# Kernel optimization log

Hardware: AMD Instinct MI355X
Metric: run time of the kernel (lower is better)

Reference implementation:

```python
import jax, jax.numpy as jnp
import numpy as np

B, N, C = 8, 1025, 768  # batch, tokens (1 CLS + 32*32 patches), channels
H = 12                  # heads
D = C // H              # head dim = 64
EPS = 1e-6

def _rot(x):
    # stack([-x[..., 1::2], x[..., ::2]], -1).reshape(x.shape)
    return jnp.stack([-x[..., 1::2], x[..., ::2]], axis=-1).reshape(x.shape)

def apply_rot_embed_cat(x, emb):
    # emb: [N-1, 2*D] = concat(sin, cos); x: [B, H, N-1, D]
    sin, cos = jnp.split(emb, 2, axis=-1)
    return x * cos + _rot(x) * sin

def setup_inputs() -> dict:
    key = jax.random.key(0)
    ks = jax.random.split(key, 8)
    s = 0.02
    return {
        "x": jax.random.normal(ks[0], (B, N, C), jnp.float32),
        "rope": jax.random.normal(ks[1], (N - 1, 2 * D), jnp.float32),
        "w_qkv": jax.random.normal(ks[2], (C, 3 * C), jnp.float32) * s,
        "q_bias": jax.random.normal(ks[3], (C,), jnp.float32) * s,
        "v_bias": jax.random.normal(ks[4], (C,), jnp.float32) * s,
        "gamma": jnp.ones((C,), jnp.float32),
        "beta": jnp.zeros((C,), jnp.float32),
        "w_proj": jax.random.normal(ks[5], (C, C), jnp.float32) * s,
        "b_proj": jnp.zeros((C,), jnp.float32),
    }

def reference(x, rope, w_qkv, q_bias, v_bias, gamma, beta, w_proj, b_proj):
    scale = D ** (-0.5)
    qkv_bias = jnp.concatenate([q_bias, jnp.zeros_like(q_bias), v_bias], axis=0)
    qkv = x @ w_qkv + qkv_bias  # [B, N, 3C]
    qkv = qkv.reshape(B, N, 3, H, D).transpose(2, 0, 3, 1, 4)  # [3, B, H, N, D]
    q, k, v = qkv[0], qkv[1], qkv[2]
    # RoPE on non-CLS tokens only
    q = jnp.concatenate([q[:, :, :1], apply_rot_embed_cat(q[:, :, 1:], rope)], axis=2)
    k = jnp.concatenate([k[:, :, :1], apply_rot_embed_cat(k[:, :, 1:], rope)], axis=2)
    attn = jnp.einsum('bhqd,bhkd->bhqk', q * scale, k)
    attn = jax.nn.softmax(attn, axis=-1)
    y = jnp.einsum('bhqk,bhkd->bhqd', attn, v)
    y = y.transpose(0, 2, 1, 3).reshape(B, N, C)
    # LayerNorm
    mu = jnp.mean(y, axis=-1, keepdims=True)
    var = jnp.mean(jnp.square(y - mu), axis=-1, keepdims=True)
    y = (y - mu) * jax.lax.rsqrt(var + EPS) * gamma + beta
    return y @ w_proj + b_proj
```

## Files before the change

### kernel.cpp

```cpp
#include <hip/hip_runtime.h>

typedef __bf16 bf16_t;
typedef __bf16 bf16x8 __attribute__((ext_vector_type(8)));
typedef float f32x4 __attribute__((ext_vector_type(4)));
typedef float f32x16 __attribute__((ext_vector_type(16)));
typedef unsigned short u16;
typedef unsigned int u32;

#define NTOK 1025
#define MTOT 8200
#define MPAD 8448
#define CDIM 768

#define GLOAD(dst, p) \
  asm volatile("global_load_dwordx4 %0, %1, off" : "=&v"(dst) : "v"((const void*)(p)))

__device__ __forceinline__ u16 f2bf(float f) {
  union { float f; unsigned u; } v; v.f = f;
  unsigned r = v.u + 0x7fffu + ((v.u >> 16) & 1u);
  return (u16)(r >> 16);
}
__device__ __forceinline__ float bf2f(u16 h) {
  union { unsigned u; float f; } v; v.u = ((unsigned)h) << 16; return v.f;
}
__device__ __forceinline__ u32 cvtpk(float lo, float hi) {
  u32 r; asm("v_cvt_pk_bf16_f32 %0, %1, %2" : "=v"(r) : "v"(lo), "v"(hi)); return r;
}

__global__ __launch_bounds__(256) void conv_xf(const float4* __restrict__ x4,
                                               u16* __restrict__ xf) {
  __shared__ u16 tile[16][776];
  int mt = blockIdx.x;
  int t = threadIdx.x;
#pragma unroll
  for (int it = 0; it < 12; ++it) {
    int id = it * 256 + t;
    int r = id / 192, c4 = id % 192;
    int m = mt * 16 + r;
    if (m < MTOT) {
      float4 f = x4[(size_t)m * 192 + c4];
      ushort4 o; o.x = f2bf(f.x); o.y = f2bf(f.y); o.z = f2bf(f.z); o.w = f2bf(f.w);
      *(ushort4*)&tile[r][c4 * 4] = o;
    }
  }
  __syncthreads();
#pragma unroll
  for (int it = 0; it < 6; ++it) {
    int cid = it * 256 + t;
    int kt = cid >> 6, lane = cid & 63;
    uint4 w = *(const uint4*)&tile[lane & 15][kt * 32 + (lane >> 4) * 8];
    *(uint4*)&xf[(((size_t)mt * 24 + kt) * 64 + lane) * 8] = w;
  }
}

__global__ __launch_bounds__(64) void transp_wf(const float* __restrict__ in, int N,
                                                u16* __restrict__ wf) {
  __shared__ u16 lds[16][32];
  int n0 = blockIdx.x * 16, k0 = blockIdx.y * 32;
  int t = threadIdx.x;
#pragma unroll
  for (int it = 0; it < 8; ++it) {
    int e = it * 64 + t;
    int kk = e >> 4, nn = e & 15;
    lds[nn][kk] = f2bf(in[(size_t)(k0 + kk) * N + n0 + nn]);
  }
  __syncthreads();
  uint4 w = *(const uint4*)&lds[t & 15][(t >> 4) * 8];
  *(uint4*)&wf[((((size_t)(n0 >> 4)) * 24 + (k0 >> 5)) * 64 + t) * 8] = w;
}

template <bool TRANS>
__device__ __forceinline__ void fdloop(const u16* __restrict__ afr, const u16* __restrict__ bfr,
                                       int m0, int n0, int lane, int wr, int wc,
                                       f32x4 (*acc)[4]) {
  const u16* ab = afr + ((size_t)((m0 >> 4) + wr * 4) * 1536 + lane) * 8;
  const u16* bb = bfr + ((size_t)((n0 >> 4) + wc * 4) * 1536 + lane) * 8;
  bf16x8 S[3][8];
  auto LOADA = [&](int s, int kt) {
#pragma unroll
    for (int i = 0; i < 4; ++i)
      GLOAD(S[s][i], ab + (size_t)i * 12288 + (size_t)kt * 512);
#pragma unroll
    for (int j = 0; j < 4; ++j)
      GLOAD(S[s][4 + j], bb + (size_t)j * 12288 + (size_t)kt * 512);
  };
  auto COMP = [&](bf16x8 (&Sc)[8]) {
    __builtin_amdgcn_s_setprio(1);
#pragma unroll
    for (int x = 0; x < 4; ++x)
#pragma unroll
      for (int y = 0; y < 4; ++y)
        acc[x][y] = TRANS
            ? __builtin_amdgcn_mfma_f32_16x16x32_bf16(Sc[4 + x], Sc[y], acc[x][y], 0, 0, 0)
            : __builtin_amdgcn_mfma_f32_16x16x32_bf16(Sc[x], Sc[4 + y], acc[x][y], 0, 0, 0);
    __builtin_amdgcn_s_setprio(0);
  };
  LOADA(0, 0);
  LOADA(1, 1);
#pragma unroll
  for (int kt = 0; kt < 24; ++kt) {
    if (kt < 22) {
      LOADA((kt + 2) % 3, kt + 2);
      asm volatile("s_waitcnt vmcnt(16)");
    } else if (kt == 22) {
      asm volatile("s_waitcnt vmcnt(8)");
    } else {
      asm volatile("s_waitcnt vmcnt(0)");
    }
    __builtin_amdgcn_sched_barrier(0);
    COMP(S[kt % 3]);
  }
}

__global__ __launch_bounds__(256, 2) void qkv_gemm_t(
    const u16* __restrict__ xf, const u16* __restrict__ wf,
    const float* __restrict__ qbias, const float* __restrict__ rope,
    u16* __restrict__ q, u16* __restrict__ kfr) {
  const int NB = 12;
  int tau0 = blockIdx.x;
  int xcd = tau0 & 7, pos = tau0 >> 3;
  int tau = (xcd < 4) ? xcd * 98 + pos : 392 + (xcd - 4) * 97 + pos;
  int bx = tau % NB, by = tau / NB;
  int m0 = by * 128, n0 = bx * 128;
  int t = threadIdx.x;
  int lane = t & 63, wave = t >> 6;
  int ln = lane & 15, hi = lane >> 4;
  int wr = wave >> 1, wc = wave & 1;

  f32x4 acc[4][4] = {};
  fdloop<true>(xf, wf, m0, n0, lane, wr, wc, acc);

  const float scale = 0.125f * 1.4426950408889634f;
#pragma unroll
  for (int ii = 0; ii < 4; ++ii) {
    int m = m0 + wr * 64 + ii * 16 + ln;
    if (m < MTOT) {
      int b = m / NTOK;
      int n = m - b * NTOK;
      const float* rp = rope + (size_t)(n - 1) * 128;
#pragma unroll
      for (int jj = 0; jj < 4; ++jj) {
        int c4 = n0 + wc * 64 + jj * 16 + hi * 4;
        int part = (c4 >= CDIM) ? 1 : 0;
        int cc = c4 - part * CDIM;
        int h = cc >> 6, d4 = cc & 63;
        float v0 = acc[jj][ii][0], v1 = acc[jj][ii][1];
        float v2 = acc[jj][ii][2], v3 = acc[jj][ii][3];
        if (part == 0) {
          float4 qb = *(const float4*)(qbias + cc);
          v0 += qb.x; v1 += qb.y; v2 += qb.z; v3 += qb.w;
        }
        float o0, o1, o2, o3;
        if (n > 0) {
          float4 sn = *(const float4*)(rp + d4);
          float4 cs = *(const float4*)(rp + 64 + d4);
          o0 = v0 * cs.x - v1 * sn.x;
          o1 = v1 * cs.y + v0 * sn.y;
          o2 = v2 * cs.z - v3 * sn.z;
          o3 = v3 * cs.w + v2 * sn.w;
        } else { o0 = v0; o1 = v1; o2 = v2; o3 = v3; }
        uint2 w;
        if (part == 0) {
          w.x = cvtpk(o0 * scale, o1 * scale); w.y = cvtpk(o2 * scale, o3 * scale);
          *(uint2*)(q + ((size_t)(h * MPAD + m)) * 64 + d4) = w;
        } else {
          w.x = cvtpk(o0, o1); w.y = cvtpk(o2, o3);
          int kt2 = n >> 5, lqn = n & 31;
          int sF = d4 >> 4, h2d = (d4 >> 3) & 1, j0 = d4 & 7;
          u16* dst = kfr + ((((size_t)(h * 8 + b) * 34 + kt2) * 4 + sF) * 64
                            + h2d * 32 + lqn) * 8 + j0;
          *(uint2*)dst = w;
        }
      }
    }
  }
}

__global__ __launch_bounds__(256, 2) void qkv_gemm_v(
    const u16* __restrict__ xf, const u16* __restrict__ wf,
    const float* __restrict__ vbias, u16* __restrict__ vfr) {
  const int NB = 6;
  int tau0 = blockIdx.x;
  int xcd = tau0 & 7, pos = tau0 >> 3;
  int tau = (xcd < 6) ? xcd * 49 + pos : 294 + (xcd - 6) * 48 + pos;
  int bx = tau % NB, by = tau / NB;
  int m0 = by * 128, n0 = 1536 + bx * 128;
  int t = threadIdx.x;
  int lane = t & 63, wave = t >> 6;
  int ln = lane & 15, hi = lane >> 4;
  int wr = wave >> 1, wc = wave & 1;

  f32x4 acc[4][4] = {};
  fdloop<false>(xf, wf, m0, n0, lane, wr, wc, acc);

#pragma unroll
  for (int i = 0; i < 4; ++i) {
    int mrow = m0 + wr * 64 + i * 16 + hi * 4;
#pragma unroll
    for (int j = 0; j < 4; ++j) {
      int cv = n0 - 1536 + wc * 64 + j * 16 + ln;
      int h = cv >> 6, d = cv & 63;
      int hf = d >> 5, lqd = d & 31;
      float vb = vbias[cv];
#pragma unroll
      for (int r = 0; r < 4; ++r) {
        int mr = mrow + r;
        if (mr < MTOT) {
          int b = mr / NTOK;
          int n = mr - b * NTOK;
          size_t idx = ((((size_t)(h * 8 + b) * 17 + (n >> 6)) * 4 + ((n >> 4) & 3)) * 2 + hf) * 512
                     + (size_t)((((n >> 3) & 1) * 32 + lqd) * 8 + (n & 7));
          vfr[idx] = f2bf(acc[i][j][r] + vb);
        }
      }
    }
  }
}

template <bool PF, bool MASK>
__device__ __forceinline__ void flash_iter(
    bf16x8 (&kf)[8], bf16x8 (&kn)[8], int pftile, int it,
    const u16* kfb, const u16* vfb, int h2,
    const bf16x8 (&qf)[4], f32x16 (&acc)[2], float& l) {
  bf16x8 vf[8];
  const u16* vp2 = vfb + (size_t)it * 4096;
#pragma unroll
  for (int hf = 0; hf < 2; ++hf)
#pragma unroll
    for (int s = 0; s < 4; ++s)
      GLOAD(vf[hf * 4 + s], vp2 + (s * 2 + hf) * 512);
  if (PF) {
    const u16* kp2 = kfb + (size_t)pftile * 4096;
#pragma unroll
    for (int c = 0; c < 2; ++c)
#pragma unroll
      for (int s = 0; s < 4; ++s)
        GLOAD(kn[c * 4 + s], kp2 + c * 2048 + s * 512);
  }
  if (PF) asm volatile("s_waitcnt vmcnt(16)");
  else    asm volatile("s_waitcnt vmcnt(8)");
  __builtin_amdgcn_sched_barrier(0);
  f32x16 sc[2] = {};
  __builtin_amdgcn_s_setprio(1);
#pragma unroll
  for (int c = 0; c < 2; ++c)
#pragma unroll
    for (int s = 0; s < 4; ++s)
      sc[c] = __builtin_amdgcn_mfma_f32_32x32x16_bf16(kf[c * 4 + s], qf[s], sc[c], 0, 0, 0);
  __builtin_amdgcn_s_setprio(0);
#pragma unroll
  for (int c = 0; c < 2; ++c)
#pragma unroll
    for (int r = 0; r < 16; ++r)
      sc[c][r] = __builtin_amdgcn_exp2f(sc[c][r]);
  if (MASK) {
#pragma unroll
    for (int c = 0; c < 2; ++c)
#pragma unroll
      for (int r = 0; r < 16; ++r) {
        int kk = it * 64 + c * 32 + (r & 3) + 8 * (r >> 2) + 4 * h2;
        if (kk >= NTOK) sc[c][r] = 0.f;
      }
  }
  float rs = 0.f;
#pragma unroll
  for (int c = 0; c < 2; ++c)
#pragma unroll
    for (int r = 0; r < 16; ++r) rs += sc[c][r];
  l += rs;
  bf16x8 frag[4];
#pragma unroll
  for (int c = 0; c < 2; ++c) {
    u32 k0 = cvtpk(sc[c][0], sc[c][1]),   k1 = cvtpk(sc[c][2], sc[c][3]);
    u32 k2 = cvtpk(sc[c][4], sc[c][5]),   k3 = cvtpk(sc[c][6], sc[c][7]);
    u32 k4 = cvtpk(sc[c][8], sc[c][9]),   k5 = cvtpk(sc[c][10], sc[c][11]);
    u32 k6 = cvtpk(sc[c][12], sc[c][13]), k7 = cvtpk(sc[c][14], sc[c][15]);
    asm("v_permlane32_swap_b32 %0, %1" : "+v"(k0), "+v"(k2));
    asm("v_permlane32_swap_b32 %0, %1" : "+v"(k1), "+v"(k3));
    asm("v_permlane32_swap_b32 %0, %1" : "+v"(k4), "+v"(k6));
    asm("v_permlane32_swap_b32 %0, %1" : "+v"(k5), "+v"(k7));
    union { u32 u[4]; bf16x8 v; } u0, u1;
    u0.u[0] = k0; u0.u[1] = k1; u0.u[2] = k2; u0.u[3] = k3;
    u1.u[0] = k4; u1.u[1] = k5; u1.u[2] = k6; u1.u[3] = k7;
    frag[c * 2] = u0.v; frag[c * 2 + 1] = u1.v;
  }
  if (PF) asm volatile("s_waitcnt vmcnt(8)");
  else    asm volatile("s_waitcnt vmcnt(0)");
  __builtin_amdgcn_sched_barrier(0);
  __builtin_amdgcn_s_setprio(1);
#pragma unroll
  for (int hf = 0; hf < 2; ++hf)
#pragma unroll
    for (int s = 0; s < 4; ++s)
      acc[hf] = __builtin_amdgcn_mfma_f32_32x32x16_bf16(vf[hf * 4 + s], frag[s], acc[hf], 0, 0, 0);
  __builtin_amdgcn_s_setprio(0);
}

__global__ __launch_bounds__(256, 2) void flash_attn(
    const u16* __restrict__ q, const u16* __restrict__ kfr,
    const u16* __restrict__ vfr, u16* __restrict__ y) {
  int f = blockIdx.x;
  int xcd = f & 7, idx = f >> 3;
  int bh = xcd * 12 + idx / 9;
  int qt = idx - (idx / 9) * 9;
  int b = bh / 12, h = bh - b * 12;
  int t = threadIdx.x, lane = t & 63, w = t >> 6;
  int lq = lane & 31, h2 = lane >> 5;
  int q0 = qt * 128 + w * 32;
  if (q0 >= NTOK) return;
  int qrow = q0 + lq; if (qrow > NTOK - 1) qrow = NTOK - 1;

  const u16* qp = q + ((size_t)(h * MPAD) + (size_t)b * NTOK + qrow) * 64;
  bf16x8 qf[4];
#pragma unroll
  for (int s = 0; s < 4; ++s)
    qf[s] = *(const bf16x8*)&qp[s * 16 + h2 * 8];

  const u16* kfb = kfr + (size_t)(h * 8 + b) * 34 * 2048 + lane * 8;
  const u16* vfb = vfr + (size_t)(h * 8 + b) * 17 * 4096 + lane * 8;

  f32x16 acc[2] = {};
  float l = 0.f;

  bf16x8 ka[8], kb2[8];
#pragma unroll
  for (int c = 0; c < 2; ++c)
#pragma unroll
    for (int s = 0; s < 4; ++s)
      GLOAD(ka[c * 4 + s], kfb + c * 2048 + s * 512);

#pragma unroll 1
  for (int i2 = 0; i2 < 8; ++i2) {
    flash_iter<true, false>(ka, kb2, 2 * i2 + 1, 2 * i2, kfb, vfb, h2, qf, acc, l);
    flash_iter<true, false>(kb2, ka, 2 * i2 + 2, 2 * i2 + 1, kfb, vfb, h2, qf, acc, l);
  }
  flash_iter<false, true>(ka, kb2, 0, 16, kfb, vfb, h2, qf, acc, l);

  int row = q0 + lq;
  if (row < NTOK) {
    float lt = l + __shfl_xor(l, 32, 64);
    float inv = 1.f / lt;
    u16* yr = y + ((size_t)(b * NTOK + row)) * CDIM + h * 64;
#pragma unroll
    for (int hf = 0; hf < 2; ++hf)
#pragma unroll
      for (int g = 0; g < 4; ++g) {
        int d0 = hf * 32 + 8 * g + 4 * h2;
        ushort4 o;
        o.x = f2bf(acc[hf][g * 4 + 0] * inv);
        o.y = f2bf(acc[hf][g * 4 + 1] * inv);
        o.z = f2bf(acc[hf][g * 4 + 2] * inv);
        o.w = f2bf(acc[hf][g * 4 + 3] * inv);
        *(ushort4*)&yr[d0] = o;
      }
  }
}

__global__ __launch_bounds__(256) void lnorm(const u16* __restrict__ y,
                                             const float* __restrict__ gamma,
                                             const float* __restrict__ beta,
                                             u16* __restrict__ yf) {
  int row = blockIdx.x;
  const u16* yr = y + (size_t)row * CDIM;
  int t = threadIdx.x;
  float v[3];
  float s = 0.f, s2 = 0.f;
#pragma unroll
  for (int i = 0; i < 3; ++i) {
    v[i] = bf2f(yr[t + 256 * i]);
    s += v[i]; s2 += v[i] * v[i];
  }
#pragma unroll
  for (int msk = 1; msk < 64; msk <<= 1) {
    s  += __shfl_xor(s, msk, 64);
    s2 += __shfl_xor(s2, msk, 64);
  }
  __shared__ float ws[8];
  int w = t >> 6, lane = t & 63;
  if (lane == 0) { ws[w] = s; ws[4 + w] = s2; }
  __syncthreads();
  s = ws[0] + ws[1] + ws[2] + ws[3];
  s2 = ws[4] + ws[5] + ws[6] + ws[7];
  float mu = s * (1.f / 768.f);
  float var = s2 * (1.f / 768.f) - mu * mu;
  float rstd = rsqrtf(var + 1e-6f);
  if (t < 96) {
    union { uint4 u4; u16 u[8]; } iv, ov;
    iv.u4 = *(const uint4*)&yr[t * 8];
    const float* gp = gamma + t * 8;
    const float* bp = beta + t * 8;
#pragma unroll
    for (int j = 0; j < 8; ++j)
      ov.u[j] = f2bf((bf2f(iv.u[j]) - mu) * rstd * gp[j] + bp[j]);
    int kt = t >> 2, ln2 = (row & 15) + 16 * (t & 3), mt = row >> 4;
    *(uint4*)&yf[(((size_t)mt * 24 + kt) * 64 + ln2) * 8] = ov.u4;
  }
}

__global__ __launch_bounds__(256, 2) void proj_gemm(
    const u16* __restrict__ yf, const u16* __restrict__ wf,
    const float* __restrict__ bias, float* __restrict__ out) {
  const int NB = 6;
  int tau0 = blockIdx.x;
  int xcd = tau0 & 7, pos = tau0 >> 3;
  int tau = (xcd < 6) ? xcd * 49 + pos : 294 + (xcd - 6) * 48 + pos;
  int bx = tau % NB, by = tau / NB;
  int m0 = by * 128, n0 = bx * 128;
  int t = threadIdx.x;
  int lane = t & 63, wave = t >> 6;
  int ln = lane & 15, hi = lane >> 4;
  int wr = wave >> 1, wc = wave & 1;

  f32x4 acc[4][4] = {};
  fdloop<true>(yf, wf, m0, n0, lane, wr, wc, acc);

#pragma unroll
  for (int ii = 0; ii < 4; ++ii) {
    int m = m0 + wr * 64 + ii * 16 + ln;
    if (m < MTOT) {
      float* dr = out + (size_t)m * CDIM;
#pragma unroll
      for (int jj = 0; jj < 4; ++jj) {
        int c4 = n0 + wc * 64 + jj * 16 + hi * 4;
        float4 bv = *(const float4*)(bias + c4);
        float4 o;
        o.x = acc[jj][ii][0] + bv.x;
        o.y = acc[jj][ii][1] + bv.y;
        o.z = acc[jj][ii][2] + bv.z;
        o.w = acc[jj][ii][3] + bv.w;
        *(float4*)(dr + c4) = o;
      }
    }
  }
}

extern "C" void kernel_launch(void* const* d_in, const int* in_sizes, int n_in,
                              void* d_out, int out_size, void* d_ws, size_t ws_size,
                              hipStream_t stream) {
  const float* x      = (const float*)d_in[0];
  const float* rope   = (const float*)d_in[1];
  const float* w_qkv  = (const float*)d_in[2];
  const float* q_bias = (const float*)d_in[3];
  const float* v_bias = (const float*)d_in[4];
  const float* gamma  = (const float*)d_in[5];
  const float* beta   = (const float*)d_in[6];
  const float* w_proj = (const float*)d_in[7];
  const float* b_proj = (const float*)d_in[8];
  float* out = (float*)d_out;

  char* ws = (char*)d_ws;
  u16* xf   = (u16*)(ws);
  u16* ybf  = (u16*)(ws);
  u16* wfq  = (u16*)(ws + 12976128);
  u16* wfp  = (u16*)(ws + 16515072);
  u16* qbuf = (u16*)(ws + 17694720);
  u16* yf   = (u16*)(ws + 17694720);
  u16* kfr  = (u16*)(ws + 30670848);
  u16* vfr  = (u16*)(ws + 44040192);

  conv_xf<<<dim3(513), 256, 0, stream>>>((const float4*)x, xf);
  transp_wf<<<dim3(144, 24), 64, 0, stream>>>(w_qkv, 2304, wfq);
  transp_wf<<<dim3(48, 24), 64, 0, stream>>>(w_proj, 768, wfp);

  qkv_gemm_t<<<dim3(780), 256, 0, stream>>>(xf, wfq, q_bias, rope, qbuf, kfr);
  qkv_gemm_v<<<dim3(390), 256, 0, stream>>>(xf, wfq, v_bias, vfr);
  flash_attn<<<dim3(864), 256, 0, stream>>>(qbuf, kfr, vfr, ybf);
  lnorm<<<8200, 256, 0, stream>>>(ybf, gamma, beta, yf);
  proj_gemm<<<dim3(390), 256, 0, stream>>>(yf, wfp, b_proj, out);
}
```

Baseline: 171.2 us.

## Merge Q/K and V projection GEMMs into one launch; use compiler-scheduled loads in flash attention

Fuses the two QKV GEMM kernels into a single 1170-block launch that branches per tile on whether it produces Q/K (with bias and RoPE) or V, with an XCD remapping for the larger grid. This removes one kernel launch and the tail imbalance between the two grids. Separately, the flash-attention loop drops its inline-asm global loads and manual vmcnt waits in favour of plain vector loads, with the K prefetch issued before the V loads. That hands scheduling to the compiler and risks losing the hand-tuned overlap of memory and MFMA.

After: 159.7 us. 6.7% less time.

```diff
diff --git a/kernel.cpp b/kernel.cpp
--- a/kernel.cpp
+++ b/kernel.cpp
@@ -112,105 +112,95 @@
   }
 }
 
-__global__ __launch_bounds__(256, 2) void qkv_gemm_t(
+__global__ __launch_bounds__(256, 2) void qkv_gemm_all(
     const u16* __restrict__ xf, const u16* __restrict__ wf,
-    const float* __restrict__ qbias, const float* __restrict__ rope,
-    u16* __restrict__ q, u16* __restrict__ kfr) {
-  const int NB = 12;
+    const float* __restrict__ qbias, const float* __restrict__ vbias,
+    const float* __restrict__ rope,
+    u16* __restrict__ q, u16* __restrict__ kfr, u16* __restrict__ vfr) {
+  const int NB = 18;
   int tau0 = blockIdx.x;
   int xcd = tau0 & 7, pos = tau0 >> 3;
-  int tau = (xcd < 4) ? xcd * 98 + pos : 392 + (xcd - 4) * 97 + pos;
+  int tau = (xcd < 2) ? xcd * 147 + pos : 294 + (xcd - 2) * 146 + pos;
   int bx = tau % NB, by = tau / NB;
-  int m0 = by * 128, n0 = bx * 128;
+  int m0 = by * 128;
   int t = threadIdx.x;
   int lane = t & 63, wave = t >> 6;
   int ln = lane & 15, hi = lane >> 4;
   int wr = wave >> 1, wc = wave & 1;
 
-  f32x4 acc[4][4] = {};
-  fdloop<true>(xf, wf, m0, n0, lane, wr, wc, acc);
-
-  const float scale = 0.125f * 1.4426950408889634f;
-#pragma unroll
-  for (int ii = 0; ii < 4; ++ii) {
-    int m = m0 + wr * 64 + ii * 16 + ln;
-    if (m < MTOT) {
-      int b = m / NTOK;
-      int n = m - b * NTOK;
-      const float* rp = rope + (size_t)(n - 1) * 128;
-#pragma unroll
-      for (int jj = 0; jj < 4; ++jj) {
-        int c4 = n0 + wc * 64 + jj * 16 + hi * 4;
-        int part = (c4 >= CDIM) ? 1 : 0;
-        int cc = c4 - part * CDIM;
-        int h = cc >> 6, d4 = cc & 63;
-        float v0 = acc[jj][ii][0], v1 = acc[jj][ii][1];
-        float v2 = acc[jj][ii][2], v3 = acc[jj][ii][3];
-        if (part == 0) {
-          float4 qb = *(const float4*)(qbias + cc);
-          v0 += qb.x; v1 += qb.y; v2 += qb.z; v3 += qb.w;
-        }
-        float o0, o1, o2, o3;
-        if (n > 0) {
-          float4 sn = *(const float4*)(rp + d4);
-          float4 cs = *(const float4*)(rp + 64 + d4);
-          o0 = v0 * cs.x - v1 * sn.x;
-          o1 = v1 * cs.y + v0 * sn.y;
-          o2 = v2 * cs.z - v3 * sn.z;
-          o3 = v3 * cs.w + v2 * sn.w;
-        } else { o0 = v0; o1 = v1; o2 = v2; o3 = v3; }
-        uint2 w;
-        if (part == 0) {
-          w.x = cvtpk(o0 * scale, o1 * scale); w.y = cvtpk(o2 * scale, o3 * scale);
-          *(uint2*)(q + ((size_t)(h * MPAD + m)) * 64 + d4) = w;
-        } else {
-          w.x = cvtpk(o0, o1); w.y = cvtpk(o2, o3);
-          int kt2 = n >> 5, lqn = n & 31;
-          int sF = d4 >> 4, h2d = (d4 >> 3) & 1, j0 = d4 & 7;
-          u16* dst = kfr + ((((size_t)(h * 8 + b) * 34 + kt2) * 4 + sF) * 64
-                            + h2d * 32 + lqn) * 8 + j0;
-          *(uint2*)dst = w;
+  if (bx < 12) {
+    int n0 = bx * 128;
+    f32x4 acc[4][4] = {};
+    fdloop<true>(xf, wf, m0, n0, lane, wr, wc, acc);
+
+    const float scale = 0.125f * 1.4426950408889634f;
+#pragma unroll
+    for (int ii = 0; ii < 4; ++ii) {
+      int m = m0 + wr * 64 + ii * 16 + ln;
+      if (m < MTOT) {
+        int b = m / NTOK;
+        int n = m - b * NTOK;
+        const float* rp = rope + (size_t)(n - 1) * 128;
+#pragma unroll
+        for (int jj = 0; jj < 4; ++jj) {
+          int c4 = n0 + wc * 64 + jj * 16 + hi * 4;
+          int part = (c4 >= CDIM) ? 1 : 0;
+          int cc = c4 - part * CDIM;
+          int h = cc >> 6, d4 = cc & 63;
+          float v0 = acc[jj][ii][0], v1 = acc[jj][ii][1];
+          float v2 = acc[jj][ii][2], v3 = acc[jj][ii][3];
+          if (part == 0) {
+            float4 qb = *(const float4*)(qbias + cc);
+            v0 += qb.x; v1 += qb.y; v2 += qb.z; v3 += qb.w;
+          }
+          float o0, o1, o2, o3;
+          if (n > 0) {
+            float4 sn = *(const float4*)(rp + d4);
+            float4 cs = *(const float4*)(rp + 64 + d4);
+            o0 = v0 * cs.x - v1 * sn.x;
+            o1 = v1 * cs.y + v0 * sn.y;
+            o2 = v2 * cs.z - v3 * sn.z;
+            o3 = v3 * cs.w + v2 * sn.w;
+          } else { o0 = v0; o1 = v1; o2 = v2; o3 = v3; }
+          uint2 w;
+          if (part == 0) {
+            w.x = cvtpk(o0 * scale, o1 * scale); w.y = cvtpk(o2 * scale, o3 * scale);
+            *(uint2*)(q + ((size_t)(h * MPAD + m)) * 64 + d4) = w;
+          } else {
+            w.x = cvtpk(o0, o1); w.y = cvtpk(o2, o3);
+            int kt2 = n >> 5, lqn = n & 31;
+            int sF = d4 >> 4, h2d = (d4 >> 3) & 1, j0 = d4 & 7;
+            u16* dst = kfr + ((((size_t)(h * 8 + b) * 34 + kt2) * 4 + sF) * 64
+                              + h2d * 32 + lqn) * 8 + j0;
+            *(uint2*)dst = w;
+          }
         }
       }
     }
-  }
-}
-
-__global__ __launch_bounds__(256, 2) void qkv_gemm_v(
-    const u16* __restrict__ xf, const u16* __restrict__ wf,
-    const float* __restrict__ vbias, u16* __restrict__ vfr) {
-  const int NB = 6;
-  int tau0 = blockIdx.x;
-  int xcd = tau0 & 7, pos = tau0 >> 3;
-  int tau = (xcd < 6) ? xcd * 49 + pos : 294 + (xcd - 6) * 48 + pos;
-  int bx = tau % NB, by = tau / NB;
-  int m0 = by * 128, n0 = 1536 + bx * 128;
-  int t = threadIdx.x;
-  int lane = t & 63, wave = t >> 6;
-  int ln = lane & 15, hi = lane >> 4;
-  int wr = wave >> 1, wc = wave & 1;
-
-  f32x4 acc[4][4] = {};
-  fdloop<false>(xf, wf, m0, n0, lane, wr, wc, acc);
-
-#pragma unroll
-  for (int i = 0; i < 4; ++i) {
-    int mrow = m0 + wr * 64 + i * 16 + hi * 4;
-#pragma unroll
-    for (int j = 0; j < 4; ++j) {
-      int cv = n0 - 1536 + wc * 64 + j * 16 + ln;
-      int h = cv >> 6, d = cv & 63;
-      int hf = d >> 5, lqd = d & 31;
-      float vb = vbias[cv];
-#pragma unroll
-      for (int r = 0; r < 4; ++r) {
-        int mr = mrow + r;
-        if (mr < MTOT) {
-          int b = mr / NTOK;
-          int n = mr - b * NTOK;
-          size_t idx = ((((size_t)(h * 8 + b) * 17 + (n >> 6)) * 4 + ((n >> 4) & 3)) * 2 + hf) * 512
-                     + (size_t)((((n >> 3) & 1) * 32 + lqd) * 8 + (n & 7));
-          vfr[idx] = f2bf(acc[i][j][r] + vb);
+  } else {
+    int n0 = 1536 + (bx - 12) * 128;
+    f32x4 acc[4][4] = {};
+    fdloop<false>(xf, wf, m0, n0, lane, wr, wc, acc);
+
+#pragma unroll
+    for (int i = 0; i < 4; ++i) {
+      int mrow = m0 + wr * 64 + i * 16 + hi * 4;
+#pragma unroll
+      for (int j = 0; j < 4; ++j) {
+        int cv = n0 - 1536 + wc * 64 + j * 16 + ln;
+        int h = cv >> 6, d = cv & 63;
+        int hf = d >> 5, lqd = d & 31;
+        float vb = vbias[cv];
+#pragma unroll
+        for (int r = 0; r < 4; ++r) {
+          int mr = mrow + r;
+          if (mr < MTOT) {
+            int b = mr / NTOK;
+            int n = mr - b * NTOK;
+            size_t idx = ((((size_t)(h * 8 + b) * 17 + (n >> 6)) * 4 + ((n >> 4) & 3)) * 2 + hf) * 512
+                       + (size_t)((((n >> 3) & 1) * 32 + lqd) * 8 + (n & 7));
+            vfr[idx] = f2bf(acc[i][j][r] + vb);
+          }
         }
       }
     }
@@ -222,24 +212,21 @@
     bf16x8 (&kf)[8], bf16x8 (&kn)[8], int pftile, int it,
     const u16* kfb, const u16* vfb, int h2,
     const bf16x8 (&qf)[4], f32x16 (&acc)[2], float& l) {
+  if (PF) {
+    const u16* kp2 = kfb + (size_t)pftile * 4096;
+#pragma unroll
+    for (int c = 0; c < 2; ++c)
+#pragma unroll
+      for (int s = 0; s < 4; ++s)
+        kn[c * 4 + s] = *(const bf16x8*)(kp2 + c * 2048 + s * 512);
+  }
   bf16x8 vf[8];
   const u16* vp2 = vfb + (size_t)it * 4096;
 #pragma unroll
   for (int hf = 0; hf < 2; ++hf)
 #pragma unroll
     for (int s = 0; s < 4; ++s)
-      GLOAD(vf[hf * 4 + s], vp2 + (s * 2 + hf) * 512);
-  if (PF) {
-    const u16* kp2 = kfb + (size_t)pftile * 4096;
-#pragma unroll
-    for (int c = 0; c < 2; ++c)
-#pragma unroll
-      for (int s = 0; s < 4; ++s)
-        GLOAD(kn[c * 4 + s], kp2 + c * 2048 + s * 512);
-  }
-  if (PF) asm volatile("s_waitcnt vmcnt(16)");
-  else    asm volatile("s_waitcnt vmcnt(8)");
-  __builtin_amdgcn_sched_barrier(0);
+      vf[hf * 4 + s] = *(const bf16x8*)(vp2 + (s * 2 + hf) * 512);
   f32x16 sc[2] = {};
   __builtin_amdgcn_s_setprio(1);
 #pragma unroll
@@ -284,9 +271,6 @@
     u1.u[0] = k4; u1.u[1] = k5; u1.u[2] = k6; u1.u[3] = k7;
     frag[c * 2] = u0.v; frag[c * 2 + 1] = u1.v;
   }
-  if (PF) asm volatile("s_waitcnt vmcnt(8)");
-  else    asm volatile("s_waitcnt vmcnt(0)");
-  __builtin_amdgcn_sched_barrier(0);
   __builtin_amdgcn_s_setprio(1);
 #pragma unroll
   for (int hf = 0; hf < 2; ++hf)
@@ -327,7 +311,7 @@
   for (int c = 0; c < 2; ++c)
 #pragma unroll
     for (int s = 0; s < 4; ++s)
-      GLOAD(ka[c * 4 + s], kfb + c * 2048 + s * 512);
+      ka[c * 4 + s] = *(const bf16x8*)(kfb + c * 2048 + s * 512);
 
 #pragma unroll 1
   for (int i2 = 0; i2 < 8; ++i2) {
@@ -462,8 +446,8 @@
   transp_wf<<<dim3(144, 24), 64, 0, stream>>>(w_qkv, 2304, wfq);
   transp_wf<<<dim3(48, 24), 64, 0, stream>>>(w_proj, 768, wfp);
 
-  qkv_gemm_t<<<dim3(780), 256, 0, stream>>>(xf, wfq, q_bias, rope, qbuf, kfr);
-  qkv_gemm_v<<<dim3(390), 256, 0, stream>>>(xf, wfq, v_bias, vfr);
+  qkv_gemm_all<<<dim3(1170), 256, 0, stream>>>(xf, wfq, q_bias, v_bias, rope,
+                                               qbuf, kfr, vfr);
   flash_attn<<<dim3(864), 256, 0, stream>>>(qbuf, kfr, vfr, ybf);
   lnorm<<<8200, 256, 0, stream>>>(ybf, gamma, beta, yf);
   proj_gemm<<<dim3(390), 256, 0, stream>>>(yf, wfp, b_proj, out);
```
